# Optimization experiments

Measured on AMD Instinct MI355X. Metric: run time of the kernel, lower is better.

## Reference

```python
import jax, jax.numpy as jnp
import numpy as np

TOP_K = 4
NORM_TOPK_PROB = False  # Qwen2-MoE default

def setup_inputs() -> dict:
    key = jax.random.key(0)
    ks = jax.random.split(key, 10)
    B, S, D = 1, 2048, 2048
    E, F, FS = 8, 1408, 5632
    s = 0.02
    return {
        "hidden_states": jax.random.normal(ks[0], (B, S, D), jnp.float32),
        "gate_w": jax.random.normal(ks[1], (E, D), jnp.float32) * s,          # router Linear weight [E, D]
        "Wg": jax.random.normal(ks[2], (E, D, F), jnp.float32) * s,           # expert gate_proj
        "Wu": jax.random.normal(ks[3], (E, D, F), jnp.float32) * s,           # expert up_proj
        "Wd": jax.random.normal(ks[4], (E, F, D), jnp.float32) * s,           # expert down_proj
        "Wsg": jax.random.normal(ks[5], (D, FS), jnp.float32) * s,            # shared gate_proj
        "Wsu": jax.random.normal(ks[6], (D, FS), jnp.float32) * s,            # shared up_proj
        "Wsd": jax.random.normal(ks[7], (FS, D), jnp.float32) * s,            # shared down_proj
        "shared_gate_w": jax.random.normal(ks[8], (D, 1), jnp.float32) * s,   # shared_expert_gate Linear(D,1)
    }

def reference(hidden_states, gate_w, Wg, Wu, Wd, Wsg, Wsu, Wsd, shared_gate_w):
    B, S, D = hidden_states.shape
    x = hidden_states.reshape(-1, D)                       # [T, D]
    T = x.shape[0]
    router_logits = x @ gate_w.T                           # [T, E]
    probs = jax.nn.softmax(router_logits.astype(jnp.float32), axis=-1)
    top_vals, top_idx = jax.lax.top_k(probs, TOP_K)        # [T, K]
    if NORM_TOPK_PROB:
        top_vals = top_vals / jnp.sum(top_vals, axis=-1, keepdims=True)
    # dense routing-weight matrix: zero for unselected experts (same math as masked naive loop)
    w = jnp.zeros_like(probs).at[jnp.arange(T)[:, None], top_idx].set(top_vals)
    w = w.astype(x.dtype)                                  # [T, E]
    # per-expert SiLU-gated MLP, computed densely over all experts
    h = jax.nn.silu(jnp.einsum('td,edf->etf', x, Wg)) * jnp.einsum('td,edf->etf', x, Wu)  # [E, T, F]
    expert_out = jnp.einsum('etf,efd->etd', h, Wd)         # [E, T, D]
    moe_out = jnp.einsum('etd,te->td', expert_out, w)      # [T, D]
    # shared expert with sigmoid gate
    shared = (jax.nn.silu(x @ Wsg) * (x @ Wsu)) @ Wsd      # [T, D]
    shared = jax.nn.sigmoid(x @ shared_gate_w) * shared    # [T,1] * [T,D]
    out = (moe_out + shared).reshape(B, S, D)
    return out, router_logits
```

## Files before the change

### kernel.cpp

```cpp
#include <hip/hip_runtime.h>
#include <hip/hip_bf16.h>

typedef __attribute__((ext_vector_type(8))) __bf16 bf16x8;
typedef __attribute__((ext_vector_type(4))) float f32x4;

#define TKN 2048
#define DMODEL 2048
#define NEXP 8
#define FEXP 1408
#define FSH 5632

__device__ __forceinline__ unsigned short f2bf(float f) {
  unsigned u = __float_as_uint(f);
  u += 0x7FFFu + ((u >> 16) & 1u);
  return (unsigned short)(u >> 16);
}
__device__ __forceinline__ unsigned pk2(float a, float b) {
  return (unsigned)f2bf(a) | ((unsigned)f2bf(b) << 16);
}

__device__ __forceinline__ void gll16(const void* g, void* l) {
  __builtin_amdgcn_global_load_lds(
      (const __attribute__((address_space(1))) unsigned*)g,
      (__attribute__((address_space(3))) unsigned*)l, 16, 0, 0);
}

enum { EPI_GU = 0, EPI_DOWN = 1, EPI_SDOWN = 2 };

__global__ __launch_bounds__(256)
void router_k(const float* __restrict__ x, const float* __restrict__ gw,
              const float* __restrict__ sgw, float* __restrict__ logits,
              float* __restrict__ sig, int* __restrict__ cnt,
              int* __restrict__ tokl, float* __restrict__ wls)
{
  const int wv = threadIdx.x >> 6, lane = threadIdx.x & 63;
  const int t = blockIdx.x * 4 + wv;
  const float* xr = x + (long)t * DMODEL;
  float xv[32];
#pragma unroll
  for (int j = 0; j < 32; j++) xv[j] = xr[lane + (j << 6)];

  float lg[8];
#pragma unroll
  for (int e = 0; e < 8; e++) {
    const float* gr = gw + (long)e * DMODEL;
    float acc = 0.f;
#pragma unroll
    for (int j = 0; j < 32; j++) acc += xv[j] * gr[lane + (j << 6)];
#pragma unroll
    for (int s = 1; s < 64; s <<= 1) acc += __shfl_xor(acc, s, 64);
    lg[e] = acc;
  }
  float sgacc = 0.f;
#pragma unroll
  for (int j = 0; j < 32; j++) sgacc += xv[j] * sgw[lane + (j << 6)];
#pragma unroll
  for (int s = 1; s < 64; s <<= 1) sgacc += __shfl_xor(sgacc, s, 64);

  if (lane == 0) {
    float mx = lg[0];
#pragma unroll
    for (int e = 1; e < 8; e++) mx = fmaxf(mx, lg[e]);
    float p[8], se = 0.f;
#pragma unroll
    for (int e = 0; e < 8; e++) { p[e] = expf(lg[e] - mx); se += p[e]; }
    float inv = 1.f / se;
#pragma unroll
    for (int e = 0; e < 8; e++) { p[e] *= inv; logits[t * 8 + e] = lg[e]; }
    sig[t] = 1.f / (1.f + expf(-sgacc));
#pragma unroll
    for (int k = 0; k < 4; k++) {
      int bi = 0; float bv = p[0];
#pragma unroll
      for (int e = 1; e < 8; e++) if (p[e] > bv) { bv = p[e]; bi = e; }
      p[bi] = -1.f;
      int pos = atomicAdd(&cnt[bi], 1);
      tokl[bi * TKN + pos] = t;
      wls[bi * TKN + pos] = bv;
    }
  }
}

__global__ void scan_k(const int* __restrict__ cnt, int* __restrict__ offs) {
  if (threadIdx.x == 0) {
    int s = 0;
    for (int e = 0; e < 8; e++) { offs[e] = s; s += cnt[e]; }
    offs[8] = s;
  }
}

__global__ __launch_bounds__(256)
void cvt_x_k(const float* __restrict__ x, char* __restrict__ xbf)
{
  long id = (long)blockIdx.x * 256 + threadIdx.x;
  int row = id >> 8, u = id & 255, kt = u >> 2, j = u & 3;
  const float* p = x + (long)row * 2048 + kt * 32 + j * 4;
  float4 a = *(const float4*)p;
  float4 b = *(const float4*)(p + 16);
  uint4 o;
  o.x = pk2(a.x, a.y); o.y = pk2(a.z, a.w);
  o.z = pk2(b.x, b.y); o.w = pk2(b.z, b.w);
  *(uint4*)(xbf + id * 16) = o;
}

__global__ __launch_bounds__(256)
void cvt_w_k(const float* __restrict__ W, long sB, int N,
             char* __restrict__ panel, long panStride)
{
  const int ct = blockIdx.x, kt = blockIdx.y, e = blockIdx.z, KT = gridDim.y;
  const float* Wp = W + (long)e * sB + (long)(kt * 32) * N + ct * 128;
  __shared__ float t[32][128];
  const int r = threadIdx.x >> 3, q = threadIdx.x & 7;
  const float* rp = Wp + (long)r * N + q * 16;
  float4 f0 = *(const float4*)(rp + 0);
  float4 f1 = *(const float4*)(rp + 4);
  float4 f2 = *(const float4*)(rp + 8);
  float4 f3 = *(const float4*)(rp + 12);
  *(float4*)&t[r][q * 16 + 0]  = f0;
  *(float4*)&t[r][q * 16 + 4]  = f1;
  *(float4*)&t[r][q * 16 + 8]  = f2;
  *(float4*)&t[r][q * 16 + 12] = f3;
  __syncthreads();
  char* outp = panel + e * panStride + ((long)ct * KT + kt) * 8192;
#pragma unroll
  for (int uu = 0; uu < 2; uu++) {
    int u = threadIdx.x + uu * 256;
    int c = u >> 2;
    int g = (u & 3) ^ ((c >> 1) & 3);
    uint4 o;
    o.x = pk2(t[g * 4 + 0][c], t[g * 4 + 1][c]);
    o.y = pk2(t[g * 4 + 2][c], t[g * 4 + 3][c]);
    o.z = pk2(t[16 + g * 4 + 0][c], t[16 + g * 4 + 1][c]);
    o.w = pk2(t[16 + g * 4 + 2][c], t[16 + g * 4 + 3][c]);
    *(uint4*)(outp + u * 16) = o;
  }
}

__global__ __launch_bounds__(256)
void cvt_gu_k(const float* __restrict__ Wg, const float* __restrict__ Wu,
              long sB, int N, char* __restrict__ panel, long panStride)
{
  const int ct = blockIdx.x, kt = blockIdx.y, e = blockIdx.z, KT = gridDim.y;
  __shared__ float t[32][128];
  const int r = threadIdx.x >> 3, q = threadIdx.x & 7;
  const float* src = ((q >> 1) & 1) ? Wu : Wg;
  const int scol = ct * 64 + ((q >> 2) << 5) + ((q & 1) << 4);
  const float* rp = src + (long)e * sB + (long)(kt * 32 + r) * N + scol;
  float4 f0 = *(const float4*)(rp + 0);
  float4 f1 = *(const float4*)(rp + 4);
  float4 f2 = *(const float4*)(rp + 8);
  float4 f3 = *(const float4*)(rp + 12);
  *(float4*)&t[r][q * 16 + 0]  = f0;
  *(float4*)&t[r][q * 16 + 4]  = f1;
  *(float4*)&t[r][q * 16 + 8]  = f2;
  *(float4*)&t[r][q * 16 + 12] = f3;
  __syncthreads();
  char* outp = panel + e * panStride + ((long)ct * KT + kt) * 8192;
#pragma unroll
  for (int uu = 0; uu < 2; uu++) {
    int u = threadIdx.x + uu * 256;
    int c = u >> 2;
    int g = (u & 3) ^ ((c >> 1) & 3);
    uint4 o;
    o.x = pk2(t[g * 4 + 0][c], t[g * 4 + 1][c]);
    o.y = pk2(t[g * 4 + 2][c], t[g * 4 + 3][c]);
    o.z = pk2(t[16 + g * 4 + 0][c], t[16 + g * 4 + 1][c]);
    o.w = pk2(t[16 + g * 4 + 2][c], t[16 + g * 4 + 3][c]);
    *(uint4*)(outp + u * 16) = o;
  }
}

template<int EPI, bool EXPERT, int KSPLIT>
__global__ __launch_bounds__(256, 4)
void gemm2_k(const char* __restrict__ Abf, long strA,
             const char* __restrict__ Bp, long sBpan, int KTtot, int NCT,
             void* __restrict__ O, int ldKo,
             const int* __restrict__ cnt, const int* __restrict__ offs,
             const int* __restrict__ tokl, const float* __restrict__ wls,
             const float* __restrict__ sig)
{
  const int tid = threadIdx.x, lane = tid & 63, w = tid >> 6;
  const int wg = blockIdx.x;

  int e = 0, rt, ct, kc = 0, M = TKN;
  if (EXPERT) {
    e = wg & 7; int q = wg >> 3; rt = q & 15; ct = q >> 4;
    M = cnt[e];
    if (rt * 128 >= M) return;
  } else {
    rt = wg & 15; int q = wg >> 4; ct = q % NCT; kc = q / NCT;
  }
  const int KT = KTtot / KSPLIT;
  const int kt0 = kc * KT;
  const int obase = EXPERT ? offs[e] : 0;

  __shared__ int s_tok[128];
  __shared__ float s_w[128];
  __shared__ alignas(16) char Ab[8192];
  __shared__ alignas(16) char Bb[8192];

  if (EXPERT) {
    if (tid < 128) {
      int r = rt * 128 + tid;
      int rc = (r < M) ? r : (M - 1);
      s_tok[tid] = tokl[e * TKN + rc];
      if (EPI == EPI_DOWN) s_w[tid] = (r < M) ? wls[e * TKN + r] : 0.f;
    }
    __syncthreads();
  }

  const int lrow0 = w * 32 + (lane >> 2);
  const int lrow1 = lrow0 + 16;
  auto rowbyte = [&](int rl) -> long {
    long gr;
    if (EPI == EPI_DOWN) { int r = rt * 128 + rl; gr = obase + ((r < M) ? r : (M - 1)); }
    else if (EXPERT)     { gr = s_tok[rl]; }
    else                 { gr = rt * 128 + rl; }
    return gr * strA;
  };
  const int au0 = (lane & 3) ^ ((lrow0 >> 1) & 3);
  const int au1 = (lane & 3) ^ ((lrow1 >> 1) & 3);
  const char* gA0 = Abf + rowbyte(lrow0) + (long)kt0 * 64 + au0 * 16;
  const char* gA1 = Abf + rowbyte(lrow1) + (long)kt0 * 64 + au1 * 16;
  const long bbase = (EXPERT ? (long)e * sBpan : 0) + ((long)ct * KTtot + kt0) * 8192
                     + w * 2048 + (long)lane * 16;
  const char* gB = Bp + bbase;

  const int wm = w >> 1, wn = w & 1, g = lane >> 4, l15 = lane & 15;
  int raOff[4], rbOff[4];
#pragma unroll
  for (int m = 0; m < 4; m++) {
    int row = wm * 64 + m * 16 + l15;
    raOff[m] = row * 64 + ((g ^ ((row >> 1) & 3)) << 4);
  }
#pragma unroll
  for (int n = 0; n < 4; n++) {
    int col = wn * 64 + n * 16 + l15;
    rbOff[n] = col * 64 + ((g ^ ((col >> 1) & 3)) << 4);
  }

  f32x4 acc[4][4] = {};

#pragma unroll 1
  for (int kt = 0; kt < KT; ++kt) {
    long ao = (long)kt * 64, bo = (long)kt * 8192;
    gll16(gA0 + ao, &Ab[w * 2048]);
    gll16(gA1 + ao, &Ab[w * 2048 + 1024]);
    gll16(gB + bo, &Bb[w * 2048]);
    gll16(gB + bo + 1024, &Bb[w * 2048 + 1024]);
    __syncthreads();

    bf16x8 av[4], bv[4];
#pragma unroll
    for (int m = 0; m < 4; m++) av[m] = *(const bf16x8*)&Ab[raOff[m]];
#pragma unroll
    for (int n = 0; n < 4; n++) bv[n] = *(const bf16x8*)&Bb[rbOff[n]];
#pragma unroll
    for (int m = 0; m < 4; m++)
#pragma unroll
      for (int n = 0; n < 4; n++)
        acc[m][n] = __builtin_amdgcn_mfma_f32_16x16x32_bf16(av[m], bv[n], acc[m][n], 0, 0, 0);
    __syncthreads();
  }

  if constexpr (EPI == EPI_GU) {
#pragma unroll
    for (int m = 0; m < 4; m++) {
#pragma unroll
      for (int n = 0; n < 2; n++) {
        int lc = ct * 64 + wn * 32 + n * 16 + l15;
        f32x4 ga = acc[m][n];
        f32x4 ua = acc[m][n + 2];
#pragma unroll
        for (int q = 0; q < 4; q++) {
          int rl = wm * 64 + m * 16 + (g << 2) + q;
          int grow = rt * 128 + rl;
          if (!EXPERT || grow < M) {
            float gv = ga[q];
            float hv = (gv / (1.f + __expf(-gv))) * ua[q];
            long byteoff = (long)(obase + grow) * ((long)ldKo * 64)
                         + (lc >> 5) * 64 + ((lc >> 2) & 3) * 16
                         + ((lc & 16) >> 1) + (lc & 3) * 2;
            *(unsigned short*)((char*)O + byteoff) = f2bf(hv);
          }
        }
      }
    }
  } else {
#pragma unroll
    for (int m = 0; m < 4; m++) {
#pragma unroll
      for (int n = 0; n < 4; n++) {
        int col = ct * 128 + wn * 64 + n * 16 + l15;
        f32x4 a = acc[m][n];
#pragma unroll
        for (int q = 0; q < 4; q++) {
          int rl = wm * 64 + m * 16 + (g << 2) + q;
          int grow = rt * 128 + rl;
          float v = a[q];
          if constexpr (EPI == EPI_DOWN) {
            if (grow < M)
              atomicAdd((float*)O + (long)s_tok[rl] * DMODEL + col, s_w[rl] * v);
          } else {
            atomicAdd((float*)O + (long)grow * DMODEL + col, sig[grow] * v);
          }
        }
      }
    }
  }
}

__device__ __forceinline__ void block_sync_fb() {
  __builtin_amdgcn_sched_barrier(0);
  asm volatile("s_waitcnt lgkmcnt(0)" ::: "memory");
  __builtin_amdgcn_s_barrier();
  __builtin_amdgcn_sched_barrier(0);
}

template<int EPI, bool EXPERT, int KSPLIT>
__global__ __launch_bounds__(256, 2)
void gemm_fb_k(const float* __restrict__ A, int lda,
               const float* __restrict__ B, const float* __restrict__ B2,
               long sB, int ldb, int Ktot,
               float* __restrict__ O, int ldo,
               const int* __restrict__ cnt, const int* __restrict__ offs,
               const int* __restrict__ tokl, const float* __restrict__ wls,
               const float* __restrict__ sig)
{
  constexpr bool FUSED = (EPI == EPI_GU);
  const int tid = threadIdx.x;
  const int lane = tid & 63;

  int e = 0, rt, kc = 0, M = TKN;
  if (EXPERT) {
    e = blockIdx.y >> 4; rt = blockIdx.y & 15;
    M = cnt[e];
    if (rt * 128 >= M) return;
  } else {
    rt = blockIdx.y & 15; kc = blockIdx.y >> 4;
  }
  const int K = Ktot / KSPLIT;
  const int koff = kc * K;
  const int colblk = blockIdx.x * 128;
  const float* Bp  = B + (EXPERT ? (long)e * sB : 0);
  const float* Bp2 = FUSED ? (B2 + (EXPERT ? (long)e * sB : 0)) : nullptr;
  const int obase = EXPERT ? offs[e] : 0;

  __shared__ alignas(16) unsigned char Ab[8192];
  __shared__ alignas(16) unsigned char Bb[8192];
  __shared__ alignas(16) unsigned char Bb2[FUSED ? 8192 : 16];
  __shared__ int s_tok[128];
  __shared__ float s_w[128];

  if (EXPERT && tid < 128) {
    int r = rt * 128 + tid;
    int rc = (r < M) ? r : (M - 1);
    s_tok[tid] = tokl[e * TKN + rc];
    if (EPI == EPI_DOWN) s_w[tid] = (r < M) ? wls[e * TKN + r] : 0.f;
  }
  if (EXPERT) __syncthreads();

  const int arowl = tid >> 1;
  const int ahalf = tid & 1;
  long arow;
  if (EPI == EPI_DOWN) {
    int r = rt * 128 + arowl;
    arow = (long)obase + ((r < M) ? r : (M - 1));
  } else if (EXPERT) {
    arow = s_tok[arowl];
  } else {
    arow = rt * 128 + arowl;
  }
  const float* aptr = A + arow * (long)lda + koff + ahalf * 16;
  int wa[4];
#pragma unroll
  for (int j = 0; j < 4; j++)
    wa[j] = arowl * 64 + ((j ^ ((arowl ^ (arowl >> 3)) & 3)) << 4) + ahalf * 8;

  const int kg = tid >> 5, ng = tid & 31;
  const float* bptr  = Bp + (long)(koff + kg * 4) * ldb + colblk + ng * 4;
  const float* bptr2 = FUSED ? (Bp2 + (long)(koff + kg * 4) * ldb + colblk + ng * 4) : nullptr;
  int wb[4];
#pragma unroll
  for (int i = 0; i < 4; i++) {
    int c = ng * 4 + i;
    wb[i] = c * 64 + ((((kg & 3) ^ ((c ^ (c >> 3)) & 3))) << 4) + (kg >> 2) * 8;
  }

  const int wid = tid >> 6, wm = wid >> 1, wn = wid & 1;
  const int g = lane >> 4, l15 = lane & 15;
  int ra[4], rb[4];
#pragma unroll
  for (int m = 0; m < 4; m++) {
    int r = wm * 64 + m * 16 + l15;
    ra[m] = r * 64 + ((g ^ ((r ^ (r >> 3)) & 3)) << 4);
  }
#pragma unroll
  for (int n = 0; n < 4; n++) {
    int c = wn * 64 + n * 16 + l15;
    rb[n] = c * 64 + ((g ^ ((c ^ (c >> 3)) & 3)) << 4);
  }

  f32x4 acc[4][4] = {};
  f32x4 acc2[4][4] = {};

  const int KT = K >> 5;
  float4 ta0[4], tb0[4], tc0[4], ta1[4], tb1[4], tc1[4];

  auto load_tile = [&](float4* ra_, float4* rb_, float4* rc_, int kt) {
    const float4* a4 = reinterpret_cast<const float4*>(aptr + kt * 32);
    ra_[0] = a4[0]; ra_[1] = a4[1]; ra_[2] = a4[2]; ra_[3] = a4[3];
    const float* bb = bptr + (long)kt * 32 * ldb;
    rb_[0] = *reinterpret_cast<const float4*>(bb);
    rb_[1] = *reinterpret_cast<const float4*>(bb + ldb);
    rb_[2] = *reinterpret_cast<const float4*>(bb + 2 * ldb);
    rb_[3] = *reinterpret_cast<const float4*>(bb + 3 * ldb);
    if (FUSED) {
      const float* cc = bptr2 + (long)kt * 32 * ldb;
      rc_[0] = *reinterpret_cast<const float4*>(cc);
      rc_[1] = *reinterpret_cast<const float4*>(cc + ldb);
      rc_[2] = *reinterpret_cast<const float4*>(cc + 2 * ldb);
      rc_[3] = *reinterpret_cast<const float4*>(cc + 3 * ldb);
    }
  };

  auto store_tile = [&](const float4* ra_, const float4* rb_, const float4* rc_) {
#pragma unroll
    for (int j = 0; j < 4; j++)
      *reinterpret_cast<uint2*>(Ab + wa[j]) =
          make_uint2(pk2(ra_[j].x, ra_[j].y), pk2(ra_[j].z, ra_[j].w));
    *reinterpret_cast<uint2*>(Bb + wb[0]) = make_uint2(pk2(rb_[0].x, rb_[1].x), pk2(rb_[2].x, rb_[3].x));
    *reinterpret_cast<uint2*>(Bb + wb[1]) = make_uint2(pk2(rb_[0].y, rb_[1].y), pk2(rb_[2].y, rb_[3].y));
    *reinterpret_cast<uint2*>(Bb + wb[2]) = make_uint2(pk2(rb_[0].z, rb_[1].z), pk2(rb_[2].z, rb_[3].z));
    *reinterpret_cast<uint2*>(Bb + wb[3]) = make_uint2(pk2(rb_[0].w, rb_[1].w), pk2(rb_[2].w, rb_[3].w));
    if (FUSED) {
      *reinterpret_cast<uint2*>(Bb2 + wb[0]) = make_uint2(pk2(rc_[0].x, rc_[1].x), pk2(rc_[2].x, rc_[3].x));
      *reinterpret_cast<uint2*>(Bb2 + wb[1]) = make_uint2(pk2(rc_[0].y, rc_[1].y), pk2(rc_[2].y, rc_[3].y));
      *reinterpret_cast<uint2*>(Bb2 + wb[2]) = make_uint2(pk2(rc_[0].z, rc_[1].z), pk2(rc_[2].z, rc_[3].z));
      *reinterpret_cast<uint2*>(Bb2 + wb[3]) = make_uint2(pk2(rc_[0].w, rc_[1].w), pk2(rc_[2].w, rc_[3].w));
    }
  };

  auto mfma_step = [&]() {
    bf16x8 av[4], bvg[4], bvu[4];
#pragma unroll
    for (int m = 0; m < 4; m++) av[m] = *reinterpret_cast<const bf16x8*>(Ab + ra[m]);
#pragma unroll
    for (int n = 0; n < 4; n++) {
      bvg[n] = *reinterpret_cast<const bf16x8*>(Bb + rb[n]);
      if (FUSED) bvu[n] = *reinterpret_cast<const bf16x8*>(Bb2 + rb[n]);
    }
#pragma unroll
    for (int m = 0; m < 4; m++)
#pragma unroll
      for (int n = 0; n < 4; n++) {
        acc[m][n] = __builtin_amdgcn_mfma_f32_16x16x32_bf16(av[m], bvg[n], acc[m][n], 0, 0, 0);
        if (FUSED)
          acc2[m][n] = __builtin_amdgcn_mfma_f32_16x16x32_bf16(av[m], bvu[n], acc2[m][n], 0, 0, 0);
      }
  };

  load_tile(ta0, tb0, tc0, 0);
#pragma unroll 1
  for (int kt = 0; kt < KT; kt += 2) {
    load_tile(ta1, tb1, tc1, kt + 1);
    store_tile(ta0, tb0, tc0);
    block_sync_fb();
    mfma_step();
    block_sync_fb();
    int k2 = (kt + 2 < KT) ? kt + 2 : 0;
    load_tile(ta0, tb0, tc0, k2);
    store_tile(ta1, tb1, tc1);
    block_sync_fb();
    mfma_step();
    block_sync_fb();
  }

#pragma unroll
  for (int m = 0; m < 4; m++) {
#pragma unroll
    for (int n = 0; n < 4; n++) {
      int col = colblk + wn * 64 + n * 16 + l15;
      f32x4 a = acc[m][n];
      f32x4 a2 = acc2[m][n];
#pragma unroll
      for (int q = 0; q < 4; q++) {
        int rl = wm * 64 + m * 16 + (g << 2) + q;
        int grow = rt * 128 + rl;
        float v = a[q];
        if (EPI == EPI_GU) {
          if (!EXPERT || grow < M) {
            float hv = (v / (1.f + __expf(-v))) * a2[q];
            O[(long)(obase + grow) * ldo + col] = hv;
          }
        } else if (EPI == EPI_DOWN) {
          if (grow < M)
            atomicAdd(&O[(long)s_tok[rl] * ldo + col], s_w[rl] * v);
        } else {
          atomicAdd(&O[(long)grow * ldo + col], sig[grow] * v);
        }
      }
    }
  }
}

extern "C" void kernel_launch(void* const* d_in, const int* in_sizes, int n_in,
                              void* d_out, int out_size, void* d_ws, size_t ws_size,
                              hipStream_t stream)
{
  (void)in_sizes; (void)n_in; (void)out_size;
  const float* x   = (const float*)d_in[0];
  const float* gw  = (const float*)d_in[1];
  const float* Wg  = (const float*)d_in[2];
  const float* Wu  = (const float*)d_in[3];
  const float* Wd  = (const float*)d_in[4];
  const float* Wsg = (const float*)d_in[5];
  const float* Wsu = (const float*)d_in[6];
  const float* Wsd = (const float*)d_in[7];
  const float* sgw = (const float*)d_in[8];

  float* out    = (float*)d_out;
  float* logits = out + (long)TKN * DMODEL;

  char* w    = (char*)d_ws;
  int*  cnt  = (int*)w;
  int*  offs = (int*)(w + 64);
  float* sig = (float*)(w + 1024);
  int*  tokl = (int*)(w + 16384);
  float* wls = (float*)(w + 81920);

  hipMemsetAsync(out, 0, (size_t)TKN * DMODEL * 4, stream);
  hipMemsetAsync(cnt, 0, 64, stream);

  router_k<<<dim3(TKN / 4), 256, 0, stream>>>(x, gw, sgw, logits, sig, cnt, tokl, wls);
  scan_k<<<1, 64, 0, stream>>>(cnt, offs);

  const size_t NEED = 241172480ull;
  if (ws_size >= NEED) {
    char* xbf     = w + 262144;
    char* h       = w + 8650752;
    char* panGUex = w + 33554432;
    char* panWd   = w + 125829120;
    char* panGUsh = w + 171966464;
    char* panWsd  = w + 218103808;
    const long sPanGU = 11534336;
    const long sPanWd = 5767168;

    cvt_x_k<<<dim3(2048), 256, 0, stream>>>(x, xbf);
    cvt_gu_k<<<dim3(22, 64, 8), 256, 0, stream>>>(Wg, Wu, (long)DMODEL * FEXP, FEXP, panGUex, sPanGU);
    cvt_w_k<<<dim3(16, 44, 8), 256, 0, stream>>>(Wd, (long)FEXP * DMODEL, DMODEL, panWd, sPanWd);
    cvt_gu_k<<<dim3(88, 64, 1), 256, 0, stream>>>(Wsg, Wsu, 0, FSH, panGUsh, 0);
    cvt_w_k<<<dim3(16, 176, 1), 256, 0, stream>>>(Wsd, 0, DMODEL, panWsd, 0);

    gemm2_k<EPI_GU, true, 1><<<dim3(8 * 16 * 22), 256, 0, stream>>>(
        xbf, 4096, panGUex, sPanGU, 64, 22, h, 44, cnt, offs, tokl, wls, nullptr);
    gemm2_k<EPI_DOWN, true, 1><<<dim3(8 * 16 * 16), 256, 0, stream>>>(
        h, 2816, panWd, sPanWd, 44, 16, out, 0, cnt, offs, tokl, wls, nullptr);
    gemm2_k<EPI_GU, false, 1><<<dim3(16 * 88), 256, 0, stream>>>(
        xbf, 4096, panGUsh, 0, 64, 88, h, 176, nullptr, nullptr, nullptr, nullptr, nullptr);
    gemm2_k<EPI_SDOWN, false, 4><<<dim3(16 * 16 * 4), 256, 0, stream>>>(
        h, 11264, panWsd, 0, 176, 16, out, 0, nullptr, nullptr, nullptr, nullptr, sig);
  } else {
    float* h = (float*)(w + (1 << 20));
    gemm_fb_k<EPI_GU, true, 1><<<dim3(FEXP / 128, 128), 256, 0, stream>>>(
        x, DMODEL, Wg, Wu, (long)DMODEL * FEXP, FEXP, DMODEL, h, FEXP, cnt, offs, tokl, wls, nullptr);
    gemm_fb_k<EPI_DOWN, true, 1><<<dim3(DMODEL / 128, 128), 256, 0, stream>>>(
        h, FEXP, Wd, nullptr, (long)FEXP * DMODEL, DMODEL, FEXP, out, DMODEL, cnt, offs, tokl, wls, nullptr);
    gemm_fb_k<EPI_GU, false, 1><<<dim3(FSH / 128, TKN / 128), 256, 0, stream>>>(
        x, DMODEL, Wsg, Wsu, 0, FSH, DMODEL, h, FSH, nullptr, nullptr, nullptr, nullptr, nullptr);
    gemm_fb_k<EPI_SDOWN, false, 4><<<dim3(DMODEL / 128, (TKN / 128) * 4), 256, 0, stream>>>(
        h, FSH, Wsd, nullptr, 0, DMODEL, FSH, out, DMODEL, nullptr, nullptr, nullptr, nullptr, sig);
  }
}
```

Measured before the change: 742.9 us.

## Use 256x256 GEMM tiles with 512 threads and double-buffered LDS

Replaces the 128x128 single-buffered bf16 MFMA GEMM with a 256x256 tile kernel run by 8 waves. Each wave computes 128x64, and global-to-LDS loads for the next k-step are issued into a second buffer while the current one is consumed. The goal is more operand reuse per loaded byte, fewer barriers stalling on loads, and fewer atomic-heavy blocks. The transpose scratch in the weight-conversion kernels is also padded to 132 columns to reduce LDS bank conflicts. In exchange, the larger tiles cut the number of blocks, which hurts load balance for the uneven per-expert token counts, and they raise register and LDS pressure (64 KB of LDS per block).

Result: slower. 957.5 us (+28.9%).

```diff
diff --git a/kernel.cpp b/kernel.cpp
--- a/kernel.cpp
+++ b/kernel.cpp
@@ -109,7 +109,7 @@
 {
   const int ct = blockIdx.x, kt = blockIdx.y, e = blockIdx.z, KT = gridDim.y;
   const float* Wp = W + (long)e * sB + (long)(kt * 32) * N + ct * 128;
-  __shared__ float t[32][128];
+  __shared__ float t[32][132];
   const int r = threadIdx.x >> 3, q = threadIdx.x & 7;
   const float* rp = Wp + (long)r * N + q * 16;
   float4 f0 = *(const float4*)(rp + 0);
@@ -141,7 +141,7 @@
               long sB, int N, char* __restrict__ panel, long panStride)
 {
   const int ct = blockIdx.x, kt = blockIdx.y, e = blockIdx.z, KT = gridDim.y;
-  __shared__ float t[32][128];
+  __shared__ float t[32][132];
   const int r = threadIdx.x >> 3, q = threadIdx.x & 7;
   const float* src = ((q >> 1) & 1) ? Wu : Wg;
   const int scol = ct * 64 + ((q >> 2) << 5) + ((q & 1) << 4);
@@ -171,37 +171,37 @@
 }
 
 template<int EPI, bool EXPERT, int KSPLIT>
-__global__ __launch_bounds__(256, 4)
-void gemm2_k(const char* __restrict__ Abf, long strA,
-             const char* __restrict__ Bp, long sBpan, int KTtot, int NCT,
-             void* __restrict__ O, int ldKo,
-             const int* __restrict__ cnt, const int* __restrict__ offs,
-             const int* __restrict__ tokl, const float* __restrict__ wls,
-             const float* __restrict__ sig)
+__global__ __launch_bounds__(512, 2)
+void gemm256_k(const char* __restrict__ Abf, long strA,
+               const char* __restrict__ Bp, long sBpan, int KTtot, int NCT,
+               void* __restrict__ O, int ldKo,
+               const int* __restrict__ cnt, const int* __restrict__ offs,
+               const int* __restrict__ tokl, const float* __restrict__ wls,
+               const float* __restrict__ sig)
 {
   const int tid = threadIdx.x, lane = tid & 63, w = tid >> 6;
   const int wg = blockIdx.x;
 
   int e = 0, rt, ct, kc = 0, M = TKN;
   if (EXPERT) {
-    e = wg & 7; int q = wg >> 3; rt = q & 15; ct = q >> 4;
+    e = wg & 7; int q = wg >> 3; rt = q & 7; ct = q >> 3;
     M = cnt[e];
-    if (rt * 128 >= M) return;
+    if (rt * 256 >= M) return;
   } else {
-    rt = wg & 15; int q = wg >> 4; ct = q % NCT; kc = q / NCT;
+    rt = wg & 7; int q = wg >> 3; ct = q % NCT; kc = q / NCT;
   }
   const int KT = KTtot / KSPLIT;
   const int kt0 = kc * KT;
   const int obase = EXPERT ? offs[e] : 0;
 
-  __shared__ int s_tok[128];
-  __shared__ float s_w[128];
-  __shared__ alignas(16) char Ab[8192];
-  __shared__ alignas(16) char Bb[8192];
+  __shared__ int s_tok[256];
+  __shared__ float s_w[256];
+  __shared__ alignas(16) char Ab[2][16384];
+  __shared__ alignas(16) char Bb[2][16384];
 
   if (EXPERT) {
-    if (tid < 128) {
-      int r = rt * 128 + tid;
+    if (tid < 256) {
+      int r = rt * 256 + tid;
       int rc = (r < M) ? r : (M - 1);
       s_tok[tid] = tokl[e * TKN + rc];
       if (EPI == EPI_DOWN) s_w[tid] = (r < M) ? wls[e * TKN + r] : 0.f;
@@ -209,29 +209,36 @@
     __syncthreads();
   }
 
-  const int lrow0 = w * 32 + (lane >> 2);
-  const int lrow1 = lrow0 + 16;
   auto rowbyte = [&](int rl) -> long {
     long gr;
-    if (EPI == EPI_DOWN) { int r = rt * 128 + rl; gr = obase + ((r < M) ? r : (M - 1)); }
+    if (EPI == EPI_DOWN) { int r = rt * 256 + rl; gr = obase + ((r < M) ? r : (M - 1)); }
     else if (EXPERT)     { gr = s_tok[rl]; }
-    else                 { gr = rt * 128 + rl; }
+    else                 { gr = rt * 256 + rl; }
     return gr * strA;
   };
-  const int au0 = (lane & 3) ^ ((lrow0 >> 1) & 3);
-  const int au1 = (lane & 3) ^ ((lrow1 >> 1) & 3);
-  const char* gA0 = Abf + rowbyte(lrow0) + (long)kt0 * 64 + au0 * 16;
-  const char* gA1 = Abf + rowbyte(lrow1) + (long)kt0 * 64 + au1 * 16;
-  const long bbase = (EXPERT ? (long)e * sBpan : 0) + ((long)ct * KTtot + kt0) * 8192
-                     + w * 2048 + (long)lane * 16;
-  const char* gB = Bp + bbase;
-
-  const int wm = w >> 1, wn = w & 1, g = lane >> 4, l15 = lane & 15;
-  int raOff[4], rbOff[4];
-#pragma unroll
-  for (int m = 0; m < 4; m++) {
-    int row = wm * 64 + m * 16 + l15;
-    raOff[m] = row * 64 + ((g ^ ((row >> 1) & 3)) << 4);
+  const int lr0 = (tid >> 2), lr1 = 128 + (tid >> 2);
+  const int u0 = (tid & 3) ^ ((lr0 >> 1) & 3);
+  const int u1 = (tid & 3) ^ ((lr1 >> 1) & 3);
+  const char* gA0 = Abf + rowbyte(lr0) + (long)kt0 * 64 + u0 * 16;
+  const char* gA1 = Abf + rowbyte(lr1) + (long)kt0 * 64 + u1 * 16;
+  const long ebase = EXPERT ? (long)e * sBpan : 0;
+  const char* gB0 = Bp + ebase + ((long)(2 * ct + 0) * KTtot + kt0) * 8192 + (long)tid * 16;
+  const char* gB1 = Bp + ebase + ((long)(2 * ct + 1) * KTtot + kt0) * 8192 + (long)tid * 16;
+
+  auto stage = [&](int bf, int kt) {
+    long ao = (long)kt * 64, bo = (long)kt * 8192;
+    gll16(gA0 + ao, &Ab[bf][w * 1024]);
+    gll16(gA1 + ao, &Ab[bf][8192 + w * 1024]);
+    gll16(gB0 + bo, &Bb[bf][w * 1024]);
+    gll16(gB1 + bo, &Bb[bf][8192 + w * 1024]);
+  };
+
+  const int wm = w >> 2, wn = w & 3, g = lane >> 4, l15 = lane & 15;
+  int raOff[8], rbOff[4];
+#pragma unroll
+  for (int mm = 0; mm < 8; mm++) {
+    int row = wm * 128 + mm * 16 + l15;
+    raOff[mm] = row * 64 + ((g ^ ((row >> 1) & 3)) << 4);
   }
 #pragma unroll
   for (int n = 0; n < 4; n++) {
@@ -239,42 +246,43 @@
     rbOff[n] = col * 64 + ((g ^ ((col >> 1) & 3)) << 4);
   }
 
-  f32x4 acc[4][4] = {};
-
+  f32x4 acc[8][4] = {};
+
+  stage(0, 0);
+  __syncthreads();
+
+  int cur = 0;
 #pragma unroll 1
   for (int kt = 0; kt < KT; ++kt) {
-    long ao = (long)kt * 64, bo = (long)kt * 8192;
-    gll16(gA0 + ao, &Ab[w * 2048]);
-    gll16(gA1 + ao, &Ab[w * 2048 + 1024]);
-    gll16(gB + bo, &Bb[w * 2048]);
-    gll16(gB + bo + 1024, &Bb[w * 2048 + 1024]);
+    if (kt + 1 < KT) stage(cur ^ 1, kt + 1);
+
+    bf16x8 av[8], bv[4];
+#pragma unroll
+    for (int mm = 0; mm < 8; mm++) av[mm] = *(const bf16x8*)&Ab[cur][raOff[mm]];
+#pragma unroll
+    for (int n = 0; n < 4; n++) bv[n] = *(const bf16x8*)&Bb[cur][rbOff[n]];
+#pragma unroll
+    for (int mm = 0; mm < 8; mm++)
+#pragma unroll
+      for (int n = 0; n < 4; n++)
+        acc[mm][n] = __builtin_amdgcn_mfma_f32_16x16x32_bf16(av[mm], bv[n], acc[mm][n], 0, 0, 0);
+
     __syncthreads();
-
-    bf16x8 av[4], bv[4];
-#pragma unroll
-    for (int m = 0; m < 4; m++) av[m] = *(const bf16x8*)&Ab[raOff[m]];
-#pragma unroll
-    for (int n = 0; n < 4; n++) bv[n] = *(const bf16x8*)&Bb[rbOff[n]];
-#pragma unroll
-    for (int m = 0; m < 4; m++)
-#pragma unroll
-      for (int n = 0; n < 4; n++)
-        acc[m][n] = __builtin_amdgcn_mfma_f32_16x16x32_bf16(av[m], bv[n], acc[m][n], 0, 0, 0);
-    __syncthreads();
+    cur ^= 1;
   }
 
   if constexpr (EPI == EPI_GU) {
 #pragma unroll
-    for (int m = 0; m < 4; m++) {
+    for (int mm = 0; mm < 8; mm++) {
 #pragma unroll
       for (int n = 0; n < 2; n++) {
-        int lc = ct * 64 + wn * 32 + n * 16 + l15;
-        f32x4 ga = acc[m][n];
-        f32x4 ua = acc[m][n + 2];
+        int lc = ct * 128 + (wn >> 1) * 64 + (wn & 1) * 32 + n * 16 + l15;
+        f32x4 ga = acc[mm][n];
+        f32x4 ua = acc[mm][n + 2];
 #pragma unroll
         for (int q = 0; q < 4; q++) {
-          int rl = wm * 64 + m * 16 + (g << 2) + q;
-          int grow = rt * 128 + rl;
+          int rl = wm * 128 + mm * 16 + (g << 2) + q;
+          int grow = rt * 256 + rl;
           if (!EXPERT || grow < M) {
             float gv = ga[q];
             float hv = (gv / (1.f + __expf(-gv))) * ua[q];
@@ -288,15 +296,15 @@
     }
   } else {
 #pragma unroll
-    for (int m = 0; m < 4; m++) {
+    for (int mm = 0; mm < 8; mm++) {
 #pragma unroll
       for (int n = 0; n < 4; n++) {
-        int col = ct * 128 + wn * 64 + n * 16 + l15;
-        f32x4 a = acc[m][n];
+        int col = ct * 256 + wn * 64 + n * 16 + l15;
+        f32x4 a = acc[mm][n];
 #pragma unroll
         for (int q = 0; q < 4; q++) {
-          int rl = wm * 64 + m * 16 + (g << 2) + q;
-          int grow = rt * 128 + rl;
+          int rl = wm * 128 + mm * 16 + (g << 2) + q;
+          int grow = rt * 256 + rl;
           float v = a[q];
           if constexpr (EPI == EPI_DOWN) {
             if (grow < M)
@@ -552,14 +560,14 @@
     cvt_gu_k<<<dim3(88, 64, 1), 256, 0, stream>>>(Wsg, Wsu, 0, FSH, panGUsh, 0);
     cvt_w_k<<<dim3(16, 176, 1), 256, 0, stream>>>(Wsd, 0, DMODEL, panWsd, 0);
 
-    gemm2_k<EPI_GU, true, 1><<<dim3(8 * 16 * 22), 256, 0, stream>>>(
-        xbf, 4096, panGUex, sPanGU, 64, 22, h, 44, cnt, offs, tokl, wls, nullptr);
-    gemm2_k<EPI_DOWN, true, 1><<<dim3(8 * 16 * 16), 256, 0, stream>>>(
-        h, 2816, panWd, sPanWd, 44, 16, out, 0, cnt, offs, tokl, wls, nullptr);
-    gemm2_k<EPI_GU, false, 1><<<dim3(16 * 88), 256, 0, stream>>>(
-        xbf, 4096, panGUsh, 0, 64, 88, h, 176, nullptr, nullptr, nullptr, nullptr, nullptr);
-    gemm2_k<EPI_SDOWN, false, 4><<<dim3(16 * 16 * 4), 256, 0, stream>>>(
-        h, 11264, panWsd, 0, 176, 16, out, 0, nullptr, nullptr, nullptr, nullptr, sig);
+    gemm256_k<EPI_GU, true, 1><<<dim3(8 * 8 * 11), 512, 0, stream>>>(
+        xbf, 4096, panGUex, sPanGU, 64, 11, h, 44, cnt, offs, tokl, wls, nullptr);
+    gemm256_k<EPI_DOWN, true, 1><<<dim3(8 * 8 * 8), 512, 0, stream>>>(
+        h, 2816, panWd, sPanWd, 44, 8, out, 0, cnt, offs, tokl, wls, nullptr);
+    gemm256_k<EPI_GU, false, 1><<<dim3(8 * 44), 512, 0, stream>>>(
+        xbf, 4096, panGUsh, 0, 64, 44, h, 176, nullptr, nullptr, nullptr, nullptr, nullptr);
+    gemm256_k<EPI_SDOWN, false, 4><<<dim3(8 * 8 * 4), 512, 0, stream>>>(
+        h, 11264, panWsd, 0, 176, 8, out, 0, nullptr, nullptr, nullptr, nullptr, sig);
   } else {
     float* h = (float*)(w + (1 << 20));
     gemm_fb_k<EPI_GU, true, 1><<<dim3(FEXP / 128, 128), 256, 0, stream>>>(
```
